# Kernel optimization log

Hardware: AMD Instinct MI355X
Metric: run time of the kernel (lower is better)

## Reference

```python
import jax, jax.numpy as jnp
import numpy as np

N, E, DIN, DE, D, L = 100000, 600000, 64, 8, 128, 5
BN_EPS = 1e-5


def setup_inputs() -> dict:
    key = jax.random.key(0)
    ks = jax.random.split(key, 10)
    s = 0.05
    return {
        "x": jax.random.normal(ks[0], (N, DIN), jnp.float32),
        "edge_index": jax.random.randint(ks[1], (2, E), 0, N, dtype=jnp.int64) if jax.config.jax_enable_x64 else jax.random.randint(ks[1], (2, E), 0, N),
        "edge_attr": jax.random.normal(ks[2], (E, DE), jnp.float32),
        "Wn": jax.random.normal(ks[3], (DIN, D), jnp.float32) * s,
        "bn0": jnp.zeros((D,), jnp.float32),
        "We": jax.random.normal(ks[4], (L, DE, D), jnp.float32) * s,
        "bee": jnp.zeros((L, D), jnp.float32),
        "W1": jax.random.normal(ks[5], (L, D, 2 * D), jnp.float32) * s,
        "b1": jnp.zeros((L, 2 * D), jnp.float32),
        "g1": jnp.ones((L, 2 * D), jnp.float32),
        "bt1": jnp.zeros((L, 2 * D), jnp.float32),
        "W2": jax.random.normal(ks[6], (L, 2 * D, D), jnp.float32) * s,
        "b2": jnp.zeros((L, D), jnp.float32),
        "eps": jnp.zeros((L,), jnp.float32),
        "gamma": jnp.ones((L, D), jnp.float32),
        "beta": jnp.zeros((L, D), jnp.float32),
    }


def _bn(z, g, b):
    # BatchNorm1d training-mode forward (biased variance over the node axis)
    mu = jnp.mean(z, axis=0)
    var = jnp.mean((z - mu) ** 2, axis=0)
    return g * (z - mu) * jax.lax.rsqrt(var + BN_EPS) + b


def reference(x, edge_index, edge_attr, Wn, bn0, We, bee, W1, b1, g1, bt1, W2, b2, eps, gamma, beta):
    h = x @ Wn + bn0  # node encoder: [N, D]
    src, dst = edge_index[0], edge_index[1]
    for l in range(L):
        ee = edge_attr @ We[l] + bee[l]              # [E, D] edge embedding
        msg = jax.nn.relu(h[src] + ee)               # gather + relu
        agg = jax.ops.segment_sum(msg, dst, num_segments=N)  # scatter-add
        z = (1.0 + eps[l]) * h + agg                 # GIN root update
        z = jax.nn.relu(_bn(z @ W1[l] + b1[l], g1[l], bt1[l]))  # MLP hidden
        z = z @ W2[l] + b2[l]                        # MLP out
        z = _bn(z, gamma[l], beta[l])                # outer BatchNorm
        if l < L - 1:
            z = jax.nn.relu(z)                       # relu on all but last layer
        h = z
    return h  # JK='last'
```

## Files before the change

### kernel.cpp

```cpp
#include <hip/hip_runtime.h>
#include <hip/hip_bf16.h>

#define N_NODES 100000
#define N_EDGES 600000
#define DIN 64
#define DE 8
#define D 128
#define TWO_D 256
#define L_LAYERS 5
#define BN_EPS 1e-5f

#define SCAN_B 256
#define SCAN_NB ((N_NODES + SCAN_B - 1) / SCAN_B)

typedef unsigned short u16;
typedef __attribute__((ext_vector_type(8))) short short8;
typedef __attribute__((ext_vector_type(4))) float f32x4;

__device__ inline u16 f2bf(float f) {
    __hip_bfloat16 h = __float2bfloat16(f);
    return *reinterpret_cast<u16*>(&h);
}
__device__ inline float bf2f(u16 u) {
    union { unsigned int i; float f; } v;
    v.i = ((unsigned int)u) << 16;
    return v.f;
}


__global__ void hist_kernel(const int* __restrict__ dst, int* __restrict__ deg) {
    int i = blockIdx.x * blockDim.x + threadIdx.x;
    if (i < N_EDGES) atomicAdd(&deg[dst[i]], 1);
}

__global__ void scan_partial_kernel(const int* __restrict__ deg, int* __restrict__ blocksum) {
    __shared__ int red[SCAN_B];
    int tid = threadIdx.x;
    int i = blockIdx.x * SCAN_B + tid;
    red[tid] = (i < N_NODES) ? deg[i] : 0;
    __syncthreads();
    for (int off = SCAN_B / 2; off > 0; off >>= 1) {
        if (tid < off) red[tid] += red[tid + off];
        __syncthreads();
    }
    if (tid == 0) blocksum[blockIdx.x] = red[0];
}

__global__ void scan_blocks_kernel(int* __restrict__ blocksum, int* __restrict__ total) {
    __shared__ int sh[512];
    int tid = threadIdx.x;
    int v = (tid < SCAN_NB) ? blocksum[tid] : 0;
    sh[tid] = v;
    __syncthreads();
    for (int off = 1; off < 512; off <<= 1) {
        int w = (tid >= off) ? sh[tid - off] : 0;
        __syncthreads();
        sh[tid] += w;
        __syncthreads();
    }
    if (tid < SCAN_NB) blocksum[tid] = sh[tid] - v;
    if (tid == 511) *total = sh[511];
}

__global__ void scan_apply_kernel(const int* __restrict__ deg, const int* __restrict__ blocksum,
                                  const int* __restrict__ total, int* __restrict__ rowptr,
                                  int* __restrict__ cursor) {
    __shared__ int sh[SCAN_B];
    int tid = threadIdx.x;
    int i = blockIdx.x * SCAN_B + tid;
    int v = (i < N_NODES) ? deg[i] : 0;
    sh[tid] = v;
    __syncthreads();
    for (int off = 1; off < SCAN_B; off <<= 1) {
        int w = (tid >= off) ? sh[tid - off] : 0;
        __syncthreads();
        sh[tid] += w;
        __syncthreads();
    }
    if (i < N_NODES) {
        int p = blocksum[blockIdx.x] + sh[tid] - v;
        rowptr[i] = p;
        cursor[i] = p;
    }
    if (i == N_NODES - 1) rowptr[N_NODES] = *total;
}

__global__ void scatter_kernel(const int* __restrict__ dst, const int* __restrict__ src,
                               int* __restrict__ cursor, int2* __restrict__ csr2) {
    int i = blockIdx.x * blockDim.x + threadIdx.x;
    if (i < N_EDGES) {
        int d = dst[i];
        int p = atomicAdd(&cursor[d], 1);
        csr2[p] = make_int2(i, src[i]);
    }
}


__global__ void prep_w_kernel(const float* __restrict__ W1, const float* __restrict__ W2,
                              const float* __restrict__ Wn, u16* __restrict__ w1t,
                              u16* __restrict__ w2t, u16* __restrict__ wnh,
                              u16* __restrict__ wnl) {
    int idx = blockIdx.x * blockDim.x + threadIdx.x;
    const int T1 = L_LAYERS * TWO_D * D;
    if (idx < T1) {
        int l = idx / (TWO_D * D);
        int rem = idx - l * (TWO_D * D);
        int n = rem >> 7;
        int k = rem & 127;
        w1t[idx] = f2bf(W1[((size_t)l * D + k) * TWO_D + n]);
    } else if (idx < 2 * T1) {
        int jdx = idx - T1;
        int l = jdx / (D * TWO_D);
        int rem = jdx - l * (D * TWO_D);
        int n = rem >> 8;
        int k = rem & 255;
        w2t[jdx] = f2bf(W2[((size_t)l * TWO_D + k) * D + n]);
    } else if (idx < 2 * T1 + D * DIN) {
        int r = idx - 2 * T1;
        int n = r >> 6;
        int k = r & 63;
        float v = Wn[(size_t)k * D + n];
        u16 hi = f2bf(v);
        wnh[r] = hi;
        wnl[r] = f2bf(v - bf2f(hi));
    }
}


__launch_bounds__(256, 4)
__global__ void encoder_kernel(const float* __restrict__ x, const u16* __restrict__ wnh,
                               const u16* __restrict__ wnl, const float* __restrict__ bn0,
                               float2* __restrict__ u2) {
    __shared__ __align__(16) u16 ENC[2 * 64 * 72];
    u16* Ah = ENC;
    u16* Al = ENC + 64 * 72;

    int tid = threadIdx.x;
    int row0 = blockIdx.x * 64;

#pragma unroll
    for (int p = 0; p < 4; p++) {
        int idx = tid + p * 256;
        int row = idx >> 4, c4 = (idx & 15) * 4;
        f32x4 v = (f32x4){0.f, 0.f, 0.f, 0.f};
        if (row0 + row < N_NODES)
            v = *(const f32x4*)(x + (size_t)(row0 + row) * DIN + c4);
        u16 hi4[4], lo4[4];
#pragma unroll
        for (int i = 0; i < 4; i++) {
            u16 hi = f2bf(v[i]);
            hi4[i] = hi;
            lo4[i] = f2bf(v[i] - bf2f(hi));
        }
        *(uint2*)(&Ah[row * 72 + c4]) = *(const uint2*)hi4;
        *(uint2*)(&Al[row * 72 + c4]) = *(const uint2*)lo4;
    }
    __syncthreads();

    int lane = tid & 63, wave = tid >> 6;
    int m16 = lane & 15, kq = lane >> 4;
    f32x4 acc[4][2];
#pragma unroll
    for (int i = 0; i < 4; i++)
#pragma unroll
        for (int c = 0; c < 2; c++) acc[i][c] = (f32x4){0.f, 0.f, 0.f, 0.f};

#pragma unroll
    for (int ks = 0; ks < 2; ks++) {
        int k0 = ks * 32 + kq * 8;
        short8 Bh[2], Bl[2];
#pragma unroll
        for (int ct = 0; ct < 2; ct++) {
            int col = ct * 64 + wave * 16 + m16;
            Bh[ct] = *(const short8*)(wnh + (size_t)col * DIN + k0);
            Bl[ct] = *(const short8*)(wnl + (size_t)col * DIN + k0);
        }
        short8 ah[4], al[4];
#pragma unroll
        for (int rt = 0; rt < 4; rt++) {
            ah[rt] = *(const short8*)(&Ah[(rt * 16 + m16) * 72 + k0]);
            al[rt] = *(const short8*)(&Al[(rt * 16 + m16) * 72 + k0]);
        }
#pragma unroll
        for (int rt = 0; rt < 4; rt++)
#pragma unroll
            for (int ct = 0; ct < 2; ct++) {
                acc[rt][ct] = __builtin_amdgcn_mfma_f32_16x16x32_bf16(ah[rt], Bh[ct],
                                                                     acc[rt][ct], 0, 0, 0);
                acc[rt][ct] = __builtin_amdgcn_mfma_f32_16x16x32_bf16(al[rt], Bh[ct],
                                                                     acc[rt][ct], 0, 0, 0);
                acc[rt][ct] = __builtin_amdgcn_mfma_f32_16x16x32_bf16(ah[rt], Bl[ct],
                                                                     acc[rt][ct], 0, 0, 0);
            }
    }

    int c = wave * 16 + m16;
    float b0 = bn0[c], b1v = bn0[64 + c];
#pragma unroll
    for (int rt = 0; rt < 4; rt++) {
#pragma unroll
        for (int rr = 0; rr < 4; rr++) {
            int row = row0 + rt * 16 + kq * 4 + rr;
            if (row < N_NODES)
                u2[(size_t)row * 64 + c] = make_float2(acc[rt][0][rr] + b0,
                                                       acc[rt][1][rr] + b1v);
        }
    }
}


__launch_bounds__(256, 4)
__global__ void front_kernel(const float* __restrict__ uPtr, const float* __restrict__ ea,
                             const int* __restrict__ rowptr_g, const int2* __restrict__ csr2,
                             const float* __restrict__ We, const float* __restrict__ bee,
                             const float* __restrict__ epsArr, int layer, int use_aff,
                             const float* __restrict__ aff2a, const float* __restrict__ aff2b,
                             const u16* __restrict__ w1t, const float* __restrict__ b1,
                             float* __restrict__ t, float* __restrict__ s1,
                             float* __restrict__ s1sq) {
    __shared__ __align__(16) u16 UNI[2 * 32 * 136];
    __shared__ float sred[512];
    __shared__ int rp[36];

    u16* Ah = UNI;
    u16* Al = UNI + 32 * 136;
    const float2* __restrict__ u2 = (const float2*)uPtr;

    int tid = threadIdx.x;
    int row0 = blockIdx.x * 32;

    if (tid < 33) {
        int g = row0 + tid;
        rp[tid] = rowptr_g[(g < N_NODES) ? g : N_NODES];
    }
    sred[tid] = 0.f;
    sred[256 + tid] = 0.f;
    __syncthreads();

    int lane = tid & 63, wave = tid >> 6;
    int j = lane;
    float epsv = 1.0f + epsArr[layer];

    float WeR[16];
#pragma unroll
    for (int k = 0; k < 8; k++) {
        WeR[2 * k] = We[k * D + j];
        WeR[2 * k + 1] = We[k * D + 64 + j];
    }
    float bee0 = bee[j], bee1 = bee[64 + j];
    float fA0 = 0.f, fA1 = 0.f, fB0 = 0.f, fB1 = 0.f;
    if (use_aff) {
        fA0 = aff2a[j]; fA1 = aff2a[64 + j];
        fB0 = aff2b[j]; fB1 = aff2b[64 + j];
    }

    {
        int wbeg = wave * 8, wend = wbeg + 8;
        int pbeg = rp[wbeg], pend = rp[wend];
        int rloc = wbeg;
        int p1c = rp[wbeg + 1];
        float acc_a = 0.f, acc_b = 0.f;
        float rCa = 0.f, rCb = 0.f, rNa = 0.f, rNb = 0.f;
        {
            int n0 = row0 + wbeg;
            if (n0 < N_NODES) {
                float2 r0 = u2[(size_t)n0 * 64 + j];
                rCa = r0.x; rCb = r0.y;
            }
            int n1 = n0 + 1;
            if (n1 < N_NODES) {
                float2 r1 = u2[(size_t)n1 * 64 + j];
                rNa = r1.x; rNb = r1.y;
            }
        }

        auto flushRow = [&]() {
            float oa = rCa, ob = rCb;
            if (use_aff) {
                oa = fmaxf(fmaf(fA0, oa, fB0), 0.f);
                ob = fmaxf(fmaf(fA1, ob, fB1), 0.f);
            }
            float za = fmaf(epsv, oa, acc_a);
            float zb = fmaf(epsv, ob, acc_b);
            u16 ha = f2bf(za), hb = f2bf(zb);
            Ah[rloc * 136 + j] = ha;
            Ah[rloc * 136 + 64 + j] = hb;
            Al[rloc * 136 + j] = f2bf(za - bf2f(ha));
            Al[rloc * 136 + 64 + j] = f2bf(zb - bf2f(hb));
            acc_a = 0.f;
            acc_b = 0.f;
            rloc++;
            rCa = rNa;
            rCb = rNb;
            if (rloc + 1 < wend) {
                int nn = row0 + rloc + 1;
                if (nn < N_NODES) {
                    float2 rn = u2[(size_t)nn * 64 + j];
                    rNa = rn.x; rNb = rn.y;
                } else {
                    rNa = 0.f; rNb = 0.f;
                }
            }
            p1c = (rloc < wend) ? rp[rloc + 1] : 0x7fffffff;
        };

        if (pbeg < pend) {
            int2 c[4];
#pragma unroll
            for (int i = 0; i < 4; i++) {
                int q = pbeg + i;
                c[i] = csr2[(q < pend) ? q : (pend - 1)];
            }
            for (int p = pbeg; p < pend; p += 4) {
                float2 v2[4];
                float4 e0[4], e1[4];
#pragma unroll
                for (int i = 0; i < 4; i++) {
                    v2[i] = u2[(size_t)c[i].y * 64 + j];
                    e0[i] = *(const float4*)(ea + (size_t)c[i].x * DE);
                    e1[i] = *(const float4*)(ea + (size_t)c[i].x * DE + 4);
                }
                int2 c2[4];
#pragma unroll
                for (int i = 0; i < 4; i++) {
                    int q = p + 4 + i;
                    c2[i] = csr2[(q < pend) ? q : (pend - 1)];
                }
#pragma unroll
                for (int i = 0; i < 4; i++) {
                    int pos = p + i;
                    if (pos < pend) {
                        while (pos >= p1c) flushRow();
                        float ha_ = v2[i].x, hb_ = v2[i].y;
                        if (use_aff) {
                            ha_ = fmaxf(fmaf(fA0, ha_, fB0), 0.f);
                            hb_ = fmaxf(fmaf(fA1, hb_, fB1), 0.f);
                        }
                        float eeA = bee0, eeB = bee1;
                        eeA = fmaf(e0[i].x, WeR[0], eeA);
                        eeB = fmaf(e0[i].x, WeR[1], eeB);
                        eeA = fmaf(e0[i].y, WeR[2], eeA);
                        eeB = fmaf(e0[i].y, WeR[3], eeB);
                        eeA = fmaf(e0[i].z, WeR[4], eeA);
                        eeB = fmaf(e0[i].z, WeR[5], eeB);
                        eeA = fmaf(e0[i].w, WeR[6], eeA);
                        eeB = fmaf(e0[i].w, WeR[7], eeB);
                        eeA = fmaf(e1[i].x, WeR[8], eeA);
                        eeB = fmaf(e1[i].x, WeR[9], eeB);
                        eeA = fmaf(e1[i].y, WeR[10], eeA);
                        eeB = fmaf(e1[i].y, WeR[11], eeB);
                        eeA = fmaf(e1[i].z, WeR[12], eeA);
                        eeB = fmaf(e1[i].z, WeR[13], eeB);
                        eeA = fmaf(e1[i].w, WeR[14], eeA);
                        eeB = fmaf(e1[i].w, WeR[15], eeB);
                        acc_a += fmaxf(ha_ + eeA, 0.f);
                        acc_b += fmaxf(hb_ + eeB, 0.f);
                    }
                }
#pragma unroll
                for (int i = 0; i < 4; i++) c[i] = c2[i];
            }
        }
        while (rloc < wend) flushRow();
    }
    __syncthreads();

    int wc = wave;
    int m16 = lane & 15, kq = lane >> 4;
    f32x4 acc[2][4];
#pragma unroll
    for (int i = 0; i < 2; i++)
#pragma unroll
        for (int c = 0; c < 4; c++) acc[i][c] = (f32x4){0.f, 0.f, 0.f, 0.f};

#pragma unroll
    for (int ks = 0; ks < 4; ks++) {
        int k0 = ks * 32 + kq * 8;
        short8 Bf[4];
#pragma unroll
        for (int ct = 0; ct < 4; ct++)
            Bf[ct] = *(const short8*)(w1t + (size_t)(wc * 64 + ct * 16 + m16) * D + k0);
        short8 ah[2], al[2];
#pragma unroll
        for (int rt = 0; rt < 2; rt++) {
            ah[rt] = *(const short8*)(&Ah[(rt * 16 + m16) * 136 + k0]);
            al[rt] = *(const short8*)(&Al[(rt * 16 + m16) * 136 + k0]);
        }
#pragma unroll
        for (int rt = 0; rt < 2; rt++)
#pragma unroll
            for (int ct = 0; ct < 4; ct++) {
                acc[rt][ct] = __builtin_amdgcn_mfma_f32_16x16x32_bf16(ah[rt], Bf[ct],
                                                                     acc[rt][ct], 0, 0, 0);
                acc[rt][ct] = __builtin_amdgcn_mfma_f32_16x16x32_bf16(al[rt], Bf[ct],
                                                                     acc[rt][ct], 0, 0, 0);
            }
    }

#pragma unroll
    for (int ct = 0; ct < 4; ct++) {
        int col = wc * 64 + ct * 16 + m16;
        float bias = b1[col];
        float ls = 0.f, lq = 0.f;
#pragma unroll
        for (int rt = 0; rt < 2; rt++) {
#pragma unroll
            for (int rr = 0; rr < 4; rr++) {
                int row = row0 + rt * 16 + kq * 4 + rr;
                if (row < N_NODES) {
                    float v = acc[rt][ct][rr] + bias;
                    __builtin_nontemporal_store(v, &t[(size_t)row * TWO_D + col]);
                    ls += v;
                    lq += v * v;
                }
            }
        }
        atomicAdd(&sred[col], ls);
        atomicAdd(&sred[256 + col], lq);
    }
    __syncthreads();
    int slot = blockIdx.x & 7;
    atomicAdd(&s1[slot * TWO_D + tid], sred[tid]);
    atomicAdd(&s1sq[slot * TWO_D + tid], sred[256 + tid]);
}


__launch_bounds__(256, 4)
__global__ void gemm2_kernel(const float* __restrict__ t, const float* __restrict__ aff1a,
                             const float* __restrict__ aff1b, const u16* __restrict__ w2t,
                             const float* __restrict__ b2, float* __restrict__ uPtr,
                             float* __restrict__ s2, float* __restrict__ s2sq) {
    __shared__ u16 CH[2 * 64 * 72];
    __shared__ float affL[512];
    __shared__ float sred[256];
    u16* AhC = CH;
    u16* AlC = CH + 64 * 72;
    float2* __restrict__ u2 = (float2*)uPtr;

    int tid = threadIdx.x;
    int row0 = blockIdx.x * 64;
    affL[tid] = aff1a[tid];
    affL[256 + tid] = aff1b[tid];
    sred[tid] = 0.f;

    int lane = tid & 63, wave = tid >> 6;
    int wc = wave;
    int m16 = lane & 15, kq = lane >> 4;
    f32x4 acc[4][2];
#pragma unroll
    for (int i = 0; i < 4; i++)
#pragma unroll
        for (int c = 0; c < 2; c++) acc[i][c] = (f32x4){0.f, 0.f, 0.f, 0.f};
    __syncthreads();

    for (int kc = 0; kc < 4; kc++) {
#pragma unroll
        for (int p = 0; p < 4; p++) {
            int idx = tid + p * 256;
            int row = idx >> 4, c4 = (idx & 15) * 4;
            f32x4 v = (f32x4){0.f, 0.f, 0.f, 0.f};
            if (row0 + row < N_NODES)
                v = *(const f32x4*)(t + (size_t)(row0 + row) * TWO_D + kc * 64 + c4);
            u16 hi4[4], lo4[4];
#pragma unroll
            for (int i = 0; i < 4; i++) {
                int k = kc * 64 + c4 + i;
                float g = fmaxf(fmaf(affL[k], v[i], affL[256 + k]), 0.f);
                u16 hi = f2bf(g);
                hi4[i] = hi;
                lo4[i] = f2bf(g - bf2f(hi));
            }
            *(uint2*)(&AhC[row * 72 + c4]) = *(const uint2*)hi4;
            *(uint2*)(&AlC[row * 72 + c4]) = *(const uint2*)lo4;
        }
        __syncthreads();
#pragma unroll
        for (int ks = 0; ks < 2; ks++) {
            int k0 = ks * 32 + kq * 8;
            short8 Bf[2];
#pragma unroll
            for (int ct = 0; ct < 2; ct++) {
                int col = ct * 64 + wc * 16 + m16;
                Bf[ct] = *(const short8*)(w2t + (size_t)col * TWO_D + kc * 64 + k0);
            }
            short8 ah[4], al[4];
#pragma unroll
            for (int rt = 0; rt < 4; rt++) {
                ah[rt] = *(const short8*)(&AhC[(rt * 16 + m16) * 72 + k0]);
                al[rt] = *(const short8*)(&AlC[(rt * 16 + m16) * 72 + k0]);
            }
#pragma unroll
            for (int rt = 0; rt < 4; rt++)
#pragma unroll
                for (int ct = 0; ct < 2; ct++) {
                    acc[rt][ct] = __builtin_amdgcn_mfma_f32_16x16x32_bf16(ah[rt], Bf[ct],
                                                                         acc[rt][ct], 0, 0, 0);
                    acc[rt][ct] = __builtin_amdgcn_mfma_f32_16x16x32_bf16(al[rt], Bf[ct],
                                                                         acc[rt][ct], 0, 0, 0);
                }
        }
        __syncthreads();
    }

    {
        int c = wc * 16 + m16;
        float biasL = b2[c], biasH = b2[c + 64];
        float lsL = 0.f, lqL = 0.f, lsH = 0.f, lqH = 0.f;
#pragma unroll
        for (int rt = 0; rt < 4; rt++) {
#pragma unroll
            for (int rr = 0; rr < 4; rr++) {
                int row = row0 + rt * 16 + kq * 4 + rr;
                if (row < N_NODES) {
                    float vL = acc[rt][0][rr] + biasL;
                    float vH = acc[rt][1][rr] + biasH;
                    u2[(size_t)row * 64 + c] = make_float2(vL, vH);
                    lsL += vL; lqL += vL * vL;
                    lsH += vH; lqH += vH * vH;
                }
            }
        }
        atomicAdd(&sred[c], lsL);
        atomicAdd(&sred[128 + c], lqL);
        atomicAdd(&sred[c + 64], lsH);
        atomicAdd(&sred[128 + c + 64], lqH);
    }
    __syncthreads();
    int slot = blockIdx.x & 7;
    if (tid < 128) atomicAdd(&s2[slot * D + tid], sred[tid]);
    else atomicAdd(&s2sq[slot * D + (tid - 128)], sred[tid]);
}


__global__ void finalize_kernel(const float* __restrict__ sums, const float* __restrict__ sumsq,
                                int ncols, const float* __restrict__ g,
                                const float* __restrict__ bt, float* __restrict__ affa,
                                float* __restrict__ affb) {
    int j = threadIdx.x;
    if (j < ncols) {
        float s = 0.f, q = 0.f;
        for (int k = 0; k < 8; k++) { s += sums[k * ncols + j]; q += sumsq[k * ncols + j]; }
        const float invN = 1.0f / (float)N_NODES;
        float mean = s * invN;
        float var = q * invN - mean * mean;
        float rstd = rsqrtf(var + BN_EPS);
        float a = g[j] * rstd;
        affa[j] = a;
        affb[j] = fmaf(-a, mean, bt[j]);
    }
}


__global__ void apply_final_kernel(const float2* __restrict__ u2, const float* __restrict__ a,
                                   const float* __restrict__ b, float* __restrict__ out) {
    const int total = N_NODES * 64;
    for (int idx = blockIdx.x * blockDim.x + threadIdx.x; idx < total;
         idx += gridDim.x * blockDim.x) {
        int n = idx >> 6, c = idx & 63;
        float2 v = u2[idx];
        out[(size_t)n * D + c] = fmaf(a[c], v.x, b[c]);
        out[(size_t)n * D + 64 + c] = fmaf(a[64 + c], v.y, b[64 + c]);
    }
}


extern "C" void kernel_launch(void* const* d_in, const int* in_sizes, int n_in,
                              void* d_out, int out_size, void* d_ws, size_t ws_size,
                              hipStream_t stream) {
    (void)in_sizes; (void)n_in; (void)out_size; (void)ws_size;
    const float* x    = (const float*)d_in[0];
    const int*   ei   = (const int*)d_in[1];
    const float* ea   = (const float*)d_in[2];
    const float* Wn   = (const float*)d_in[3];
    const float* bn0  = (const float*)d_in[4];
    const float* We   = (const float*)d_in[5];
    const float* bee  = (const float*)d_in[6];
    const float* W1   = (const float*)d_in[7];
    const float* b1   = (const float*)d_in[8];
    const float* g1   = (const float*)d_in[9];
    const float* bt1  = (const float*)d_in[10];
    const float* W2   = (const float*)d_in[11];
    const float* b2   = (const float*)d_in[12];
    const float* eps  = (const float*)d_in[13];
    const float* gamma= (const float*)d_in[14];
    const float* beta = (const float*)d_in[15];
    float* out = (float*)d_out;

    char* ws = (char*)d_ws;
    float* u      = (float*)ws;
    float* t      = (float*)(ws + 51200000);
    int*   rowptr = (int*)(ws + 153600000);
    int*   deg    = (int*)(ws + 154000004);
    int*   cursor = (int*)(ws + 154400004);
    int*   blocksum = (int*)(ws + 154800004);
    int*   totalp = blocksum + SCAN_NB;
    int2*  csr2   = (int2*)(ws + 154801584);
    float* stats  = (float*)(ws + 159601840);
    float* s1    = stats;
    float* s1sq  = stats + 2048;
    float* s2    = stats + 4096;
    float* s2sq  = stats + 5120;
    float* aff1a = stats + 6144;
    float* aff1b = stats + 6400;
    float* aff2a = stats + 6656;
    float* aff2b = stats + 6784;
    u16*   w1t   = (u16*)(ws + 159629504);
    u16*   w2t   = (u16*)(ws + 154000016);
    u16*   wnh   = (u16*)(ws + 154400016);
    u16*   wnl   = (u16*)(ws + 154416400);

    const int* srcA = ei;
    const int* dstA = ei + N_EDGES;

    (void)hipMemsetAsync(deg, 0, N_NODES * sizeof(int), stream);
    (void)hipMemsetAsync(csr2 + N_EDGES, 0, 32 * sizeof(int2), stream);
    hist_kernel<<<(N_EDGES + 255) / 256, 256, 0, stream>>>(dstA, deg);
    scan_partial_kernel<<<SCAN_NB, SCAN_B, 0, stream>>>(deg, blocksum);
    scan_blocks_kernel<<<1, 512, 0, stream>>>(blocksum, totalp);
    scan_apply_kernel<<<SCAN_NB, SCAN_B, 0, stream>>>(deg, blocksum, totalp, rowptr, cursor);
    scatter_kernel<<<(N_EDGES + 255) / 256, 256, 0, stream>>>(dstA, srcA, cursor, csr2);

    const int PREP_T = 2 * L_LAYERS * TWO_D * D + D * DIN;
    prep_w_kernel<<<(PREP_T + 255) / 256, 256, 0, stream>>>(W1, W2, Wn, w1t, w2t, wnh, wnl);
    encoder_kernel<<<(N_NODES + 63) / 64, 256, 0, stream>>>(x, wnh, wnl, bn0, (float2*)u);

    const int NB1 = (N_NODES + 31) / 32;
    const int NB2 = (N_NODES + 63) / 64;
    for (int l = 0; l < L_LAYERS; l++) {
        (void)hipMemsetAsync(stats, 0, 6144 * sizeof(float), stream);
        front_kernel<<<NB1, 256, 0, stream>>>(
            u, ea, rowptr, csr2, We + (size_t)l * DE * D, bee + (size_t)l * D,
            eps, l, (l > 0) ? 1 : 0, aff2a, aff2b,
            w1t + (size_t)l * TWO_D * D, b1 + (size_t)l * TWO_D, t, s1, s1sq);
        finalize_kernel<<<1, 256, 0, stream>>>(s1, s1sq, TWO_D, g1 + (size_t)l * TWO_D,
                                               bt1 + (size_t)l * TWO_D, aff1a, aff1b);
        gemm2_kernel<<<NB2, 256, 0, stream>>>(
            t, aff1a, aff1b, w2t + (size_t)l * D * TWO_D, b2 + (size_t)l * D, u, s2, s2sq);
        finalize_kernel<<<1, 128, 0, stream>>>(s2, s2sq, D, gamma + (size_t)l * D,
                                               beta + (size_t)l * D, aff2a, aff2b);
    }
    apply_final_kernel<<<4096, 256, 0, stream>>>((const float2*)u, aff2a, aff2b, out);
}
```

Measured before the change: 1.192 ms.

## Double-buffer edge gathers and scalarize CSR descriptors in front kernel

```diff
diff --git a/kernel.cpp b/kernel.cpp
--- a/kernel.cpp
+++ b/kernel.cpp
@@ -209,7 +209,7 @@
 }
 
 
-__launch_bounds__(256, 4)
+__launch_bounds__(256, 3)
 __global__ void front_kernel(const float* __restrict__ uPtr, const float* __restrict__ ea,
                              const int* __restrict__ rowptr_g, const int2* __restrict__ csr2,
                              const float* __restrict__ We, const float* __restrict__ bee,
@@ -256,9 +256,10 @@
 
     {
         int wbeg = wave * 8, wend = wbeg + 8;
-        int pbeg = rp[wbeg], pend = rp[wend];
+        int pbeg = __builtin_amdgcn_readfirstlane(rp[wbeg]);
+        int pend = __builtin_amdgcn_readfirstlane(rp[wend]);
         int rloc = wbeg;
-        int p1c = rp[wbeg + 1];
+        int p1c = __builtin_amdgcn_readfirstlane(rp[wbeg + 1]);
         float acc_a = 0.f, acc_b = 0.f;
         float rCa = 0.f, rCb = 0.f, rNa = 0.f, rNb = 0.f;
         {
@@ -301,67 +302,84 @@
                     rNa = 0.f; rNb = 0.f;
                 }
             }
-            p1c = (rloc < wend) ? rp[rloc + 1] : 0x7fffffff;
+            p1c = (rloc < wend) ? __builtin_amdgcn_readfirstlane(rp[rloc + 1]) : 0x7fffffff;
         };
 
+#define LOAD_DESC(BASE, CC)                                                       \
+        _Pragma("unroll")                                                         \
+        for (int i_ = 0; i_ < 4; i_++) {                                          \
+            int q_ = (BASE) + i_;                                                 \
+            int2 d_ = csr2[(q_ < pend) ? q_ : (pend - 1)];                        \
+            CC##e[i_] = __builtin_amdgcn_readfirstlane(d_.x);                     \
+            CC##s[i_] = __builtin_amdgcn_readfirstlane(d_.y);                     \
+        }
+
+#define ISSUE_DATA(CC, V, E0, E1)                                                 \
+        _Pragma("unroll")                                                         \
+        for (int i_ = 0; i_ < 4; i_++) {                                          \
+            V[i_] = u2[(size_t)CC##s[i_] * 64 + j];                               \
+            const float4* pe_ = (const float4*)(ea + (size_t)CC##e[i_] * DE);     \
+            E0[i_] = pe_[0];                                                      \
+            E1[i_] = pe_[1];                                                      \
+        }
+
+#define COMPUTE_CHUNK(P, V, E0, E1)                                               \
+        _Pragma("unroll")                                                         \
+        for (int i_ = 0; i_ < 4; i_++) {                                          \
+            int pos_ = (P) + i_;                                                  \
+            if (pos_ < pend) {                                                    \
+                while (pos_ >= p1c) flushRow();                                   \
+                float ha_ = V[i_].x, hb_ = V[i_].y;                               \
+                if (use_aff) {                                                    \
+                    ha_ = fmaxf(fmaf(fA0, ha_, fB0), 0.f);                        \
+                    hb_ = fmaxf(fmaf(fA1, hb_, fB1), 0.f);                        \
+                }                                                                 \
+                float eeA = bee0, eeB = bee1;                                     \
+                eeA = fmaf(E0[i_].x, WeR[0], eeA);                                \
+                eeB = fmaf(E0[i_].x, WeR[1], eeB);                                \
+                eeA = fmaf(E0[i_].y, WeR[2], eeA);                                \
+                eeB = fmaf(E0[i_].y, WeR[3], eeB);                                \
+                eeA = fmaf(E0[i_].z, WeR[4], eeA);                                \
+                eeB = fmaf(E0[i_].z, WeR[5], eeB);                                \
+                eeA = fmaf(E0[i_].w, WeR[6], eeA);                                \
+                eeB = fmaf(E0[i_].w, WeR[7], eeB);                                \
+                eeA = fmaf(E1[i_].x, WeR[8], eeA);                                \
+                eeB = fmaf(E1[i_].x, WeR[9], eeB);                                \
+                eeA = fmaf(E1[i_].y, WeR[10], eeA);                               \
+                eeB = fmaf(E1[i_].y, WeR[11], eeB);                               \
+                eeA = fmaf(E1[i_].z, WeR[12], eeA);                               \
+                eeB = fmaf(E1[i_].z, WeR[13], eeB);                               \
+                eeA = fmaf(E1[i_].w, WeR[14], eeA);                               \
+                eeB = fmaf(E1[i_].w, WeR[15], eeB);                               \
+                acc_a += fmaxf(ha_ + eeA, 0.f);                                   \
+                acc_b += fmaxf(hb_ + eeB, 0.f);                                   \
+            }                                                                     \
+        }
+
         if (pbeg < pend) {
-            int2 c[4];
-#pragma unroll
-            for (int i = 0; i < 4; i++) {
-                int q = pbeg + i;
-                c[i] = csr2[(q < pend) ? q : (pend - 1)];
-            }
-            for (int p = pbeg; p < pend; p += 4) {
-                float2 v2[4];
-                float4 e0[4], e1[4];
-#pragma unroll
-                for (int i = 0; i < 4; i++) {
-                    v2[i] = u2[(size_t)c[i].y * 64 + j];
-                    e0[i] = *(const float4*)(ea + (size_t)c[i].x * DE);
-                    e1[i] = *(const float4*)(ea + (size_t)c[i].x * DE + 4);
-                }
-                int2 c2[4];
-#pragma unroll
-                for (int i = 0; i < 4; i++) {
-                    int q = p + 4 + i;
-                    c2[i] = csr2[(q < pend) ? q : (pend - 1)];
-                }
-#pragma unroll
-                for (int i = 0; i < 4; i++) {
-                    int pos = p + i;
-                    if (pos < pend) {
-                        while (pos >= p1c) flushRow();
-                        float ha_ = v2[i].x, hb_ = v2[i].y;
-                        if (use_aff) {
-                            ha_ = fmaxf(fmaf(fA0, ha_, fB0), 0.f);
-                            hb_ = fmaxf(fmaf(fA1, hb_, fB1), 0.f);
-                        }
-                        float eeA = bee0, eeB = bee1;
-                        eeA = fmaf(e0[i].x, WeR[0], eeA);
-                        eeB = fmaf(e0[i].x, WeR[1], eeB);
-                        eeA = fmaf(e0[i].y, WeR[2], eeA);
-                        eeB = fmaf(e0[i].y, WeR[3], eeB);
-                        eeA = fmaf(e0[i].z, WeR[4], eeA);
-                        eeB = fmaf(e0[i].z, WeR[5], eeB);
-                        eeA = fmaf(e0[i].w, WeR[6], eeA);
-                        eeB = fmaf(e0[i].w, WeR[7], eeB);
-                        eeA = fmaf(e1[i].x, WeR[8], eeA);
-                        eeB = fmaf(e1[i].x, WeR[9], eeB);
-                        eeA = fmaf(e1[i].y, WeR[10], eeA);
-                        eeB = fmaf(e1[i].y, WeR[11], eeB);
-                        eeA = fmaf(e1[i].z, WeR[12], eeA);
-                        eeB = fmaf(e1[i].z, WeR[13], eeB);
-                        eeA = fmaf(e1[i].w, WeR[14], eeA);
-                        eeB = fmaf(e1[i].w, WeR[15], eeB);
-                        acc_a += fmaxf(ha_ + eeA, 0.f);
-                        acc_b += fmaxf(hb_ + eeB, 0.f);
-                    }
-                }
-#pragma unroll
-                for (int i = 0; i < 4; i++) c[i] = c2[i];
+            int cAe[4], cAs[4], cBe[4], cBs[4], cNe[4], cNs[4], cMe[4], cMs[4];
+            float2 vA[4], vB[4];
+            float4 eA0[4], eA1[4], eB0[4], eB1[4];
+
+            LOAD_DESC(pbeg, cA)
+            LOAD_DESC(pbeg + 4, cB)
+            ISSUE_DATA(cA, vA, eA0, eA1)
+            ISSUE_DATA(cB, vB, eB0, eB1)
+            LOAD_DESC(pbeg + 8, cN)
+            for (int p = pbeg; p < pend; p += 8) {
+                LOAD_DESC(p + 12, cM)
+                COMPUTE_CHUNK(p, vA, eA0, eA1)
+                ISSUE_DATA(cN, vA, eA0, eA1)
+                LOAD_DESC(p + 16, cN)
+                COMPUTE_CHUNK(p + 4, vB, eB0, eB1)
+                ISSUE_DATA(cM, vB, eB0, eB1)
             }
         }
         while (rloc < wend) flushRow();
+
+#undef LOAD_DESC
+#undef ISSUE_DATA
+#undef COMPUTE_CHUNK
     }
     __syncthreads();
 
```

Measured after the change: 1.067 ms. 1.12x faster.
